# Kernel tuning notes

Hardware: AMD Instinct MI355X
Metric: run time of the kernel (lower is better)

The kernel has to match this reference:

```python
import jax, jax.numpy as jnp
import numpy as np

B, S, D, H = 2, 2048, 1024, 16
DH = D // H
EPS = 1e-5


def _ln(x, g, b):
    m = jnp.mean(x, axis=-1, keepdims=True)
    v = jnp.mean((x - m) ** 2, axis=-1, keepdims=True)
    return (x - m) * jax.lax.rsqrt(v + EPS) * g + b


def setup_inputs() -> dict:
    key = jax.random.key(0)
    ks = jax.random.split(key, 16)
    w = lambda k, shp: jax.random.normal(k, shp, jnp.float32) * 0.02
    return {
        "x": jax.random.normal(ks[0], (B, S, D), jnp.float32),
        # semantic preprocessor: Linear(D,2D) -> ReLU -> Linear(2D,D), residual + LN
        "pW1": w(ks[1], (D, 2 * D)), "pb1": jnp.zeros((2 * D,), jnp.float32),
        "pW2": w(ks[2], (2 * D, D)), "pb2": jnp.zeros((D,), jnp.float32),
        "gp": jnp.ones((D,), jnp.float32), "bp": jnp.zeros((D,), jnp.float32),
        # multi-head attention projections
        "Wq": w(ks[3], (D, D)), "bq": jnp.zeros((D,), jnp.float32),
        "Wk": w(ks[4], (D, D)), "bk": jnp.zeros((D,), jnp.float32),
        "Wv": w(ks[5], (D, D)), "bv": jnp.zeros((D,), jnp.float32),
        "Wo": w(ks[6], (D, D)), "bo": jnp.zeros((D,), jnp.float32),
        "g1": jnp.ones((D,), jnp.float32), "b1": jnp.zeros((D,), jnp.float32),
        # FFN: Linear(D,4D) -> ReLU -> Linear(4D,D)
        "Wf1": w(ks[7], (D, 4 * D)), "bf1": jnp.zeros((4 * D,), jnp.float32),
        "Wf2": w(ks[8], (4 * D, D)), "bf2": jnp.zeros((D,), jnp.float32),
        "g2": jnp.ones((D,), jnp.float32), "b2": jnp.zeros((D,), jnp.float32),
    }


def reference(x, pW1, pb1, pW2, pb2, gp, bp,
              Wq, bq, Wk, bk, Wv, bv, Wo, bo, g1, b1,
              Wf1, bf1, Wf2, bf2, g2, b2):
    # specialized 'semantic' preprocessor (dropout = identity in eval)
    h = jax.nn.relu(x @ pW1 + pb1) @ pW2 + pb2
    s = _ln(x + h, gp, bp)                       # [B,S,D]
    # naive multi-head attention
    q = (s @ Wq + bq).reshape(B, S, H, DH)
    k = (s @ Wk + bk).reshape(B, S, H, DH)
    v = (s @ Wv + bv).reshape(B, S, H, DH)
    scores = jnp.einsum("bqhd,bkhd->bhqk", q, k) / np.sqrt(DH).astype(np.float32)
    attn = jax.nn.softmax(scores, axis=-1)       # [B,H,S,S]
    ctx = jnp.einsum("bhqk,bkhd->bqhd", attn, v).reshape(B, S, D)
    attn_out = ctx @ Wo + bo
    y = _ln(s + attn_out, g1, b1)
    # FFN (dropouts = identity)
    f = jax.nn.relu(y @ Wf1 + bf1) @ Wf2 + bf2
    return _ln(y + f, g2, b2)
```

## Files before the change

kernel.cpp:

```cpp
#include <hip/hip_runtime.h>
#include <cstdint>
#include <cstddef>

typedef _Float16 f16;
typedef _Float16 f16x8 __attribute__((ext_vector_type(8)));
typedef _Float16 f16x4 __attribute__((ext_vector_type(4)));
typedef float    f32x4 __attribute__((ext_vector_type(4)));
typedef float    f32x16 __attribute__((ext_vector_type(16)));

#define MFMA16(a,b,c) __builtin_amdgcn_mfma_f32_16x16x32_f16(a, b, c, 0, 0, 0)
#define MFMA32(a,b,c) __builtin_amdgcn_mfma_f32_32x32x16_f16(a, b, c, 0, 0, 0)

static __device__ __forceinline__ void gload_lds16(const void* g, void* l) {
  __builtin_amdgcn_global_load_lds(
      (const __attribute__((address_space(1))) unsigned int*)g,
      (__attribute__((address_space(3))) unsigned int*)l, 16, 0, 0);
}

static __device__ __forceinline__ int pkh(float a, float b) {
  auto t = __builtin_amdgcn_cvt_pkrtz(a, b);
  return __builtin_bit_cast(int, t);
}

static __device__ __forceinline__ float ex2(float x) {
  return __builtin_amdgcn_exp2f(x);
}

__global__ __launch_bounds__(256) void cast_kernel(const float* __restrict__ x,
                                                   f16* __restrict__ y, int n4) {
  int i = blockIdx.x * 256 + threadIdx.x;
  if (i < n4) {
    float4 v = ((const float4*)x)[i];
    f16x4 h;
    h[0] = (f16)v.x; h[1] = (f16)v.y; h[2] = (f16)v.z; h[3] = (f16)v.w;
    *(f16x4*)(y + (size_t)i * 4) = h;
  }
}

__global__ __launch_bounds__(256) void wtrans(const float* __restrict__ W,
                                              f16* __restrict__ Wt, int K, int N,
                                              float scale) {
  __shared__ float tile[32][33];
  const int n0 = blockIdx.x * 32, k0 = blockIdx.y * 32;
  const int c = threadIdx.x & 31, r = threadIdx.x >> 5;
#pragma unroll
  for (int i = 0; i < 4; i++) {
    int row = r + i * 8;
    tile[row][c] = W[(size_t)(k0 + row) * N + n0 + c];
  }
  __syncthreads();
#pragma unroll
  for (int i = 0; i < 4; i++) {
    int row = r + i * 8;
    Wt[(size_t)(n0 + row) * K + k0 + c] = (f16)(tile[c][row] * scale);
  }
}

__global__ __launch_bounds__(256) void qkvbias_kernel(const float* __restrict__ bq,
                                                      const float* __restrict__ bk,
                                                      const float* __restrict__ bv,
                                                      float* __restrict__ bqkv) {
  int i = blockIdx.x * 256 + threadIdx.x;
  if (i < 1024)       bqkv[i] = bq[i] * 0.18033688f;
  else if (i < 2048)  bqkv[i] = bk[i - 1024];
  else if (i < 3072)  bqkv[i] = bv[i - 2048];
}

template <int MODE, int BN>
__global__ __launch_bounds__(256, 2)
void gemm_kernel(const f16* __restrict__ A, const f16* __restrict__ W,
                 const float* __restrict__ bias, const float* __restrict__ res,
                 void* __restrict__ out, f16* __restrict__ vt, int N, int K) {
  __shared__ __align__(16) f16 lsA[128 * 64];
  __shared__ __align__(16) f16 lsB[BN * 64];
  constexpr int MI = (BN == 128) ? 4 : 2;
  constexpr int NB = (BN == 128) ? 4 : 2;
  const int tid  = threadIdx.x;
  const int lane = tid & 63;
  const int wid  = tid >> 6;
  const int frow = lane & 15;
  const int kgrp = lane >> 4;
  const int wmBase = (BN == 128) ? (wid >> 1) * 64 : wid * 32;
  const int wnBase = (BN == 128) ? (wid & 1) * 64 : 0;
  const int bn = blockIdx.x, bm = blockIdx.y;

  const f32x4 zero4 = {0.f, 0.f, 0.f, 0.f};
  f32x4 acc[MI][4];
#pragma unroll
  for (int i = 0; i < MI; i++)
#pragma unroll
    for (int j = 0; j < 4; j++) acc[i][j] = zero4;

  const f16* aSrc[4]; int lOffA[4];
  const f16* bSrc[NB]; int lOffB[NB];
#pragma unroll
  for (int i = 0; i < 4; i++) {
    int c_lin = i * 256 + wid * 64 + lane;
    int row = c_lin >> 3;
    int ch  = (c_lin & 7) ^ (row & 7);
    aSrc[i] = A + (size_t)(bm * 128 + row) * K + ch * 8;
    lOffA[i] = (i * 256 + wid * 64) * 8;
  }
#pragma unroll
  for (int i = 0; i < NB; i++) {
    int c_lin = i * 256 + wid * 64 + lane;
    int row = c_lin >> 3;
    int ch  = (c_lin & 7) ^ (row & 7);
    bSrc[i] = W + (size_t)(bn * BN + row) * K + ch * 8;
    lOffB[i] = (i * 256 + wid * 64) * 8;
  }

  const int nk = K >> 6;
  for (int ks = 0; ks < nk; ++ks) {
#pragma unroll
    for (int i = 0; i < 4; i++) gload_lds16(aSrc[i] + ks * 64, &lsA[lOffA[i]]);
#pragma unroll
    for (int i = 0; i < NB; i++) gload_lds16(bSrc[i] + ks * 64, &lsB[lOffB[i]]);
    __syncthreads();
#pragma unroll
    for (int kk = 0; kk < 2; kk++) {
      f16x8 af[MI], bf[4];
#pragma unroll
      for (int i = 0; i < MI; i++) {
        int row = wmBase + i * 16 + frow;
        af[i] = *(const f16x8*)&lsA[row * 64 + (((kk * 4 + kgrp) ^ (row & 7)) << 3)];
      }
#pragma unroll
      for (int j = 0; j < 4; j++) {
        int row = wnBase + j * 16 + frow;
        bf[j] = *(const f16x8*)&lsB[row * 64 + (((kk * 4 + kgrp) ^ (row & 7)) << 3)];
      }
#pragma unroll
      for (int i = 0; i < MI; i++)
#pragma unroll
        for (int j = 0; j < 4; j++) acc[i][j] = MFMA16(af[i], bf[j], acc[i][j]);
    }
    __syncthreads();
  }

#pragma unroll
  for (int j = 0; j < 4; j++) {
    const int col = bn * BN + wnBase + j * 16 + frow;
    const float bb = bias[col];
#pragma unroll
    for (int i = 0; i < MI; i++) {
      const int row0 = bm * 128 + wmBase + i * 16 + kgrp * 4;
      if (MODE == 3 && col >= 2048) {
        const int vcol = col - 2048;
        const int bh = (row0 >> 11) * 16 + (vcol >> 6);
        const int d  = vcol & 63;
        const int kv = row0 & 2047;
        f16x4 pk;
#pragma unroll
        for (int r = 0; r < 4; r++) pk[r] = (f16)(acc[i][j][r] + bb);
        *(f16x4*)(vt + ((size_t)bh * 64 + d) * 2048 + kv) = pk;
      } else {
#pragma unroll
        for (int r = 0; r < 4; r++) {
          float v = acc[i][j][r] + bb;
          const size_t idx = (size_t)(row0 + r) * N + col;
          if (MODE == 1) v = fmaxf(v, 0.f);
          if (MODE == 2) ((float*)out)[idx] = v + res[idx];
          else           ((f16*)out)[idx]   = (f16)v;
        }
      }
    }
  }
}

__global__ __launch_bounds__(256, 2)
void attn_kernel(const f16* __restrict__ Qp, const f16* __restrict__ Kp,
                 const f16* __restrict__ Vt, f16* __restrict__ Op, int ldq) {
  __shared__ __align__(16) f16 lsKb[2 * 64 * 64];
  __shared__ __align__(16) f16 lsVb[2 * 64 * 64];
  const int tid = threadIdx.x, lane = tid & 63, wid = tid >> 6;
  const int qcol = lane & 31;
  const int hi = lane >> 5;
  const int bid = blockIdx.x;
  const int bh = ((bid & 7) << 2) | ((bid >> 3) & 3);
  const int qt = bid >> 5;
  const int b = bh >> 4, h = bh & 15;
  const size_t rb = (size_t)b * 2048;
  const int hc = h * 64;
  const int qrow = qt * 128 + wid * 32 + qcol;

  f16x8 qf[4];
  {
    const f16* qp = Qp + (rb + qrow) * ldq + hc;
#pragma unroll
    for (int kc = 0; kc < 4; kc++) qf[kc] = *(const f16x8*)(qp + kc * 16 + hi * 8);
  }

  f32x16 ot0, ot1;
#pragma unroll
  for (int i = 0; i < 16; i++) { ot0[i] = 0.f; ot1[i] = 0.f; }
  float mrun = -1e30f, lrun = 0.f;

  const f16 *kS0, *kS1, *vS0, *vS1;
  int off0, off1;
  {
    int c0 = wid * 64 + lane;
    int r0 = c0 >> 3, ch0 = (c0 & 7) ^ (r0 & 7);
    int c1 = 256 + wid * 64 + lane;
    int r1 = c1 >> 3, ch1 = (c1 & 7) ^ (r1 & 7);
    kS0 = Kp + (rb + r0) * ldq + hc + ch0 * 8;
    kS1 = Kp + (rb + r1) * ldq + hc + ch1 * 8;
    const f16* vbase = Vt + (size_t)bh * 64 * 2048;
    vS0 = vbase + (size_t)r0 * 2048 + ch0 * 8;
    vS1 = vbase + (size_t)r1 * 2048 + ch1 * 8;
    off0 = (wid * 64) * 8;
    off1 = (256 + wid * 64) * 8;
  }

#define STAGE(T, PB)                                                     \
  {                                                                      \
    f16* kd = lsKb + (PB) * 4096;                                        \
    f16* vd = lsVb + (PB) * 4096;                                        \
    const size_t ko = (size_t)(T) * 64 * ldq;                            \
    const size_t vo = (size_t)(T) * 64;                                  \
    gload_lds16(kS0 + ko, kd + off0);                                    \
    gload_lds16(kS1 + ko, kd + off1);                                    \
    gload_lds16(vS0 + vo, vd + off0);                                    \
    gload_lds16(vS1 + vo, vd + off1);                                    \
  }

  STAGE(0, 0);
  asm volatile("s_waitcnt vmcnt(0)" ::: "memory");
  __builtin_amdgcn_s_barrier();

  for (int kt = 0; kt < 32; ++kt) {
    const int cur = kt & 1;
    if (kt < 31) STAGE(kt + 1, cur ^ 1);
    const f16* kb = lsKb + cur * 4096;
    const f16* vb = lsVb + cur * 4096;

#pragma unroll
    for (int st = 0; st < 2; ++st) {
      f32x16 sa;
#pragma unroll
      for (int i = 0; i < 16; i++) sa[i] = 0.f;
      const int krow = st * 32 + qcol;
#pragma unroll
      for (int kc = 0; kc < 4; kc++) {
        f16x8 ak = *(const f16x8*)&kb[krow * 64 + (((kc * 2 + hi) ^ (krow & 7)) << 3)];
        sa = MFMA32(ak, qf[kc], sa);
      }

      float pr[16];
#pragma unroll
      for (int r = 0; r < 16; r++) pr[r] = sa[r];
      float pmax = pr[0];
#pragma unroll
      for (int r = 1; r < 16; r++) pmax = fmaxf(pmax, pr[r]);
      pmax = fmaxf(pmax, __shfl_xor(pmax, 32));
      if (__any(pmax > mrun + 11.54f)) {
        float mn = fmaxf(mrun, pmax);
        float fac = ex2(mrun - mn);
        mrun = mn;
        lrun *= fac;
#pragma unroll
        for (int i = 0; i < 16; i++) { ot0[i] *= fac; ot1[i] *= fac; }
      }
      float ps = 0.f;
#pragma unroll
      for (int r = 0; r < 16; r++) { pr[r] = ex2(pr[r] - mrun); ps += pr[r]; }
      ps += __shfl_xor(ps, 32);
      lrun += ps;

#pragma unroll
      for (int c0 = 0; c0 < 2; c0++) {
        const int c8 = c0 * 8;
        int a0 = pkh(pr[c8 + 0], pr[c8 + 1]);
        int a1 = pkh(pr[c8 + 2], pr[c8 + 3]);
        int b0 = pkh(pr[c8 + 4], pr[c8 + 5]);
        int b1 = pkh(pr[c8 + 6], pr[c8 + 7]);
        int sa0 = __shfl_xor(a0, 32), sb0 = __shfl_xor(b0, 32);
        int sa1 = __shfl_xor(a1, 32), sb1 = __shfl_xor(b1, 32);
        int4 wv;
        wv.x = hi ? sb0 : a0;
        wv.y = hi ? sb1 : a1;
        wv.z = hi ? b0 : sa0;
        wv.w = hi ? b1 : sa1;
        f16x8 pfrag = __builtin_bit_cast(f16x8, wv);
        const int ch = st * 4 + c0 * 2 + hi;
        {
          const int vr = qcol;
          f16x8 av = *(const f16x8*)&vb[vr * 64 + ((ch ^ (vr & 7)) << 3)];
          ot0 = MFMA32(av, pfrag, ot0);
        }
        {
          const int vr = 32 + qcol;
          f16x8 av = *(const f16x8*)&vb[vr * 64 + ((ch ^ (vr & 7)) << 3)];
          ot1 = MFMA32(av, pfrag, ot1);
        }
      }
    }
    asm volatile("s_waitcnt vmcnt(0)" ::: "memory");
    __builtin_amdgcn_s_barrier();
  }
#undef STAGE

  const float rinv = 1.f / lrun;
  f16* op = Op + (rb + qrow) * 1024 + hc;
#pragma unroll
  for (int rr = 0; rr < 16; rr += 2) {
    const int d = (rr & 3) + 8 * (rr >> 2) + 4 * hi;
    *(int*)(op + d)      = pkh(ot0[rr] * rinv, ot0[rr + 1] * rinv);
    *(int*)(op + 32 + d) = pkh(ot1[rr] * rinv, ot1[rr + 1] * rinv);
  }
}

__global__ __launch_bounds__(256)
void ln_kernel(const float* __restrict__ x, const float* __restrict__ g,
               const float* __restrict__ be, float* __restrict__ of,
               f16* __restrict__ ob) {
  const int row = blockIdx.x, t = threadIdx.x;
  const float4 v = ((const float4*)(x + (size_t)row * 1024))[t];
  float s = v.x + v.y + v.z + v.w;
  float q = v.x * v.x + v.y * v.y + v.z * v.z + v.w * v.w;
#pragma unroll
  for (int off = 1; off < 64; off <<= 1) {
    s += __shfl_xor(s, off);
    q += __shfl_xor(q, off);
  }
  __shared__ float ss[4], sq[4];
  if ((t & 63) == 0) { ss[t >> 6] = s; sq[t >> 6] = q; }
  __syncthreads();
  s = ss[0] + ss[1] + ss[2] + ss[3];
  q = sq[0] + sq[1] + sq[2] + sq[3];
  const float mean = s * (1.f / 1024.f);
  const float var  = q * (1.f / 1024.f) - mean * mean;
  const float rstd = rsqrtf(var + 1e-5f);
  const float4 gv = ((const float4*)g)[t];
  const float4 bv = ((const float4*)be)[t];
  float4 ov;
  ov.x = (v.x - mean) * rstd * gv.x + bv.x;
  ov.y = (v.y - mean) * rstd * gv.y + bv.y;
  ov.z = (v.z - mean) * rstd * gv.z + bv.z;
  ov.w = (v.w - mean) * rstd * gv.w + bv.w;
  if (of) ((float4*)(of + (size_t)row * 1024))[t] = ov;
  if (ob) {
    f16x4 hv;
    hv[0] = (f16)ov.x; hv[1] = (f16)ov.y; hv[2] = (f16)ov.z; hv[3] = (f16)ov.w;
    *(f16x4*)(ob + (size_t)row * 1024 + t * 4) = hv;
  }
}

extern "C" void kernel_launch(void* const* d_in, const int* in_sizes, int n_in,
                              void* d_out, int out_size, void* d_ws, size_t ws_size,
                              hipStream_t stream) {
  const float* x   = (const float*)d_in[0];
  const float* pW1 = (const float*)d_in[1];
  const float* pb1 = (const float*)d_in[2];
  const float* pW2 = (const float*)d_in[3];
  const float* pb2 = (const float*)d_in[4];
  const float* gp  = (const float*)d_in[5];
  const float* bp  = (const float*)d_in[6];
  const float* Wq  = (const float*)d_in[7];
  const float* bq  = (const float*)d_in[8];
  const float* Wk  = (const float*)d_in[9];
  const float* bk  = (const float*)d_in[10];
  const float* Wv  = (const float*)d_in[11];
  const float* bv  = (const float*)d_in[12];
  const float* Wo  = (const float*)d_in[13];
  const float* bo  = (const float*)d_in[14];
  const float* g1  = (const float*)d_in[15];
  const float* b1  = (const float*)d_in[16];
  const float* Wf1 = (const float*)d_in[17];
  const float* bf1 = (const float*)d_in[18];
  const float* Wf2 = (const float*)d_in[19];
  const float* bf2 = (const float*)d_in[20];
  const float* g2  = (const float*)d_in[21];
  const float* b2  = (const float*)d_in[22];

  char* ws = (char*)d_ws;
  const size_t MB = 1024 * 1024;
  if (ws_size < 121 * MB) return;

  f16*   wtP1 = (f16*)(ws);
  f16*   wtP2 = (f16*)(ws + 4 * MB);
  f16*   wtQ  = (f16*)(ws + 8 * MB);
  f16*   wtK  = (f16*)(ws + 10 * MB);
  f16*   wtV  = (f16*)(ws + 12 * MB);
  f16*   wtO  = (f16*)(ws + 14 * MB);
  f16*   wtF1 = (f16*)(ws + 16 * MB);
  f16*   wtF2 = (f16*)(ws + 24 * MB);
  f16*   big  = (f16*)(ws + 32 * MB);
  float* t32  = (float*)(ws + 64 * MB);
  float* s32  = (float*)(ws + 80 * MB);
  float* y32  = (float*)(ws + 96 * MB);
  f16*   ybuf = (f16*)(ws + 112 * MB);
  float* bqkv = (float*)(ws + 120 * MB);
  f16* xb  = (f16*)t32;
  f16* sb  = (f16*)y32;
  f16* ctx = ybuf;
  f16* Vt  = big + (size_t)4096 * 3072;

  dim3 blk(256);
  qkvbias_kernel<<<12, blk, 0, stream>>>(bq, bk, bv, bqkv);
  cast_kernel<<<4096, blk, 0, stream>>>(x, xb, 1048576);
  wtrans<<<dim3(64, 32),  blk, 0, stream>>>(pW1, wtP1, 1024, 2048, 1.f);
  wtrans<<<dim3(32, 64),  blk, 0, stream>>>(pW2, wtP2, 2048, 1024, 1.f);
  wtrans<<<dim3(32, 32),  blk, 0, stream>>>(Wq,  wtQ,  1024, 1024, 0.18033688f);
  wtrans<<<dim3(32, 32),  blk, 0, stream>>>(Wk,  wtK,  1024, 1024, 1.f);
  wtrans<<<dim3(32, 32),  blk, 0, stream>>>(Wv,  wtV,  1024, 1024, 1.f);
  wtrans<<<dim3(32, 32),  blk, 0, stream>>>(Wo,  wtO,  1024, 1024, 1.f);
  wtrans<<<dim3(128, 32), blk, 0, stream>>>(Wf1, wtF1, 1024, 4096, 1.f);
  wtrans<<<dim3(32, 128), blk, 0, stream>>>(Wf2, wtF2, 4096, 1024, 1.f);

  gemm_kernel<1,128><<<dim3(16, 32), blk, 0, stream>>>(xb, wtP1, pb1, nullptr, big, nullptr, 2048, 1024);
  gemm_kernel<2,64><<<dim3(16, 32), blk, 0, stream>>>(big, wtP2, pb2, x, t32, nullptr, 1024, 2048);
  ln_kernel<<<4096, blk, 0, stream>>>(t32, gp, bp, s32, sb);
  gemm_kernel<3,128><<<dim3(24, 32), blk, 0, stream>>>(sb, wtQ, bqkv, nullptr, big, Vt, 3072, 1024);
  attn_kernel<<<512, blk, 0, stream>>>(big, big + 1024, Vt, ctx, 3072);
  gemm_kernel<2,64><<<dim3(16, 32), blk, 0, stream>>>(ctx, wtO, bo, s32, t32, nullptr, 1024, 1024);
  ln_kernel<<<4096, blk, 0, stream>>>(t32, g1, b1, y32, ybuf);
  gemm_kernel<1,128><<<dim3(32, 32), blk, 0, stream>>>(ybuf, wtF1, bf1, nullptr, big, nullptr, 4096, 1024);
  gemm_kernel<2,64><<<dim3(16, 32), blk, 0, stream>>>(big, wtF2, bf2, y32, t32, nullptr, 1024, 4096);
  ln_kernel<<<4096, blk, 0, stream>>>(t32, g2, b2, (float*)d_out, nullptr);
}
```

Measured before the change: 321.2 us.

## Double-buffer GEMM LDS loads, deepen attention prefetch, remap workgroups across XCDs

The GEMM kernel now double-buffers its LDS tiles. It issues the global-to-LDS loads for the next K step before computing the current one and uses partial vmcnt waits instead of two full syncthreads per step. The attention kernel moves from two to four K/V LDS buffers with a prefetch distance of two tiles, and MFMA sections are wrapped in s_setprio. GEMM launches switch to a 1D grid whose block index is remapped so that neighbouring tiles land on the same XCD. In exchange, LDS use per block doubles, which may lower occupancy, and redundant tail loads are issued.

```diff
diff --git a/kernel.cpp b/kernel.cpp
--- a/kernel.cpp
+++ b/kernel.cpp
@@ -70,11 +70,12 @@
 __global__ __launch_bounds__(256, 2)
 void gemm_kernel(const f16* __restrict__ A, const f16* __restrict__ W,
                  const float* __restrict__ bias, const float* __restrict__ res,
-                 void* __restrict__ out, f16* __restrict__ vt, int N, int K) {
-  __shared__ __align__(16) f16 lsA[128 * 64];
-  __shared__ __align__(16) f16 lsB[BN * 64];
+                 void* __restrict__ out, f16* __restrict__ vt, int N, int K,
+                 int gx) {
+  constexpr int NB = (BN == 128) ? 4 : 2;
   constexpr int MI = (BN == 128) ? 4 : 2;
-  constexpr int NB = (BN == 128) ? 4 : 2;
+  __shared__ __align__(16) f16 lsA[2 * 128 * 64];
+  __shared__ __align__(16) f16 lsB[2 * BN * 64];
   const int tid  = threadIdx.x;
   const int lane = tid & 63;
   const int wid  = tid >> 6;
@@ -82,7 +83,10 @@
   const int kgrp = lane >> 4;
   const int wmBase = (BN == 128) ? (wid >> 1) * 64 : wid * 32;
   const int wnBase = (BN == 128) ? (wid & 1) * 64 : 0;
-  const int bn = blockIdx.x, bm = blockIdx.y;
+
+  const int nwg = gridDim.x;
+  const int wg = (blockIdx.x & 7) * (nwg >> 3) + (blockIdx.x >> 3);
+  const int bm = wg / gx, bn = wg % gx;
 
   const f32x4 zero4 = {0.f, 0.f, 0.f, 0.f};
   f32x4 acc[MI][4];
@@ -110,33 +114,53 @@
     lOffB[i] = (i * 256 + wid * 64) * 8;
   }
 
+#define GSTAGE(T, PB)                                                     \
+  {                                                                       \
+    f16* la = lsA + (PB) * (128 * 64);                                    \
+    f16* lb = lsB + (PB) * (BN * 64);                                     \
+    _Pragma("unroll") for (int i = 0; i < 4; i++)                         \
+      gload_lds16(aSrc[i] + (size_t)(T) * 64, la + lOffA[i]);             \
+    _Pragma("unroll") for (int i = 0; i < NB; i++)                        \
+      gload_lds16(bSrc[i] + (size_t)(T) * 64, lb + lOffB[i]);             \
+  }
+
   const int nk = K >> 6;
+  GSTAGE(0, 0);
   for (int ks = 0; ks < nk; ++ks) {
-#pragma unroll
-    for (int i = 0; i < 4; i++) gload_lds16(aSrc[i] + ks * 64, &lsA[lOffA[i]]);
-#pragma unroll
-    for (int i = 0; i < NB; i++) gload_lds16(bSrc[i] + ks * 64, &lsB[lOffB[i]]);
-    __syncthreads();
+    const int nt = (ks + 1 < nk) ? ks + 1 : nk - 1;
+    GSTAGE(nt, (ks + 1) & 1);
+    if constexpr (BN == 128)
+      asm volatile("s_waitcnt vmcnt(8)" ::: "memory");
+    else
+      asm volatile("s_waitcnt vmcnt(6)" ::: "memory");
+    __builtin_amdgcn_s_barrier();
+    const f16* la = lsA + (ks & 1) * (128 * 64);
+    const f16* lb = lsB + (ks & 1) * (BN * 64);
 #pragma unroll
     for (int kk = 0; kk < 2; kk++) {
       f16x8 af[MI], bf[4];
 #pragma unroll
       for (int i = 0; i < MI; i++) {
         int row = wmBase + i * 16 + frow;
-        af[i] = *(const f16x8*)&lsA[row * 64 + (((kk * 4 + kgrp) ^ (row & 7)) << 3)];
+        af[i] = *(const f16x8*)&la[row * 64 + (((kk * 4 + kgrp) ^ (row & 7)) << 3)];
       }
 #pragma unroll
       for (int j = 0; j < 4; j++) {
         int row = wnBase + j * 16 + frow;
-        bf[j] = *(const f16x8*)&lsB[row * 64 + (((kk * 4 + kgrp) ^ (row & 7)) << 3)];
-      }
+        bf[j] = *(const f16x8*)&lb[row * 64 + (((kk * 4 + kgrp) ^ (row & 7)) << 3)];
+      }
+      __builtin_amdgcn_s_setprio(1);
 #pragma unroll
       for (int i = 0; i < MI; i++)
 #pragma unroll
         for (int j = 0; j < 4; j++) acc[i][j] = MFMA16(af[i], bf[j], acc[i][j]);
+      __builtin_amdgcn_s_setprio(0);
     }
-    __syncthreads();
-  }
+    asm volatile("" ::: "memory");
+    __builtin_amdgcn_s_barrier();
+  }
+#undef GSTAGE
+  asm volatile("s_waitcnt vmcnt(0)" ::: "memory");
 
 #pragma unroll
   for (int j = 0; j < 4; j++) {
@@ -171,8 +195,8 @@
 __global__ __launch_bounds__(256, 2)
 void attn_kernel(const f16* __restrict__ Qp, const f16* __restrict__ Kp,
                  const f16* __restrict__ Vt, f16* __restrict__ Op, int ldq) {
-  __shared__ __align__(16) f16 lsKb[2 * 64 * 64];
-  __shared__ __align__(16) f16 lsVb[2 * 64 * 64];
+  __shared__ __align__(16) f16 lsKb[4 * 64 * 64];
+  __shared__ __align__(16) f16 lsVb[4 * 64 * 64];
   const int tid = threadIdx.x, lane = tid & 63, wid = tid >> 6;
   const int qcol = lane & 31;
   const int hi = lane >> 5;
@@ -212,7 +236,7 @@
     off1 = (256 + wid * 64) * 8;
   }
 
-#define STAGE(T, PB)                                                     \
+#define ASTAGE(T, PB)                                                    \
   {                                                                      \
     f16* kd = lsKb + (PB) * 4096;                                        \
     f16* vd = lsVb + (PB) * 4096;                                        \
@@ -224,15 +248,16 @@
     gload_lds16(vS1 + vo, vd + off1);                                    \
   }
 
-  STAGE(0, 0);
-  asm volatile("s_waitcnt vmcnt(0)" ::: "memory");
-  __builtin_amdgcn_s_barrier();
+  ASTAGE(0, 0);
+  ASTAGE(1, 1);
 
   for (int kt = 0; kt < 32; ++kt) {
-    const int cur = kt & 1;
-    if (kt < 31) STAGE(kt + 1, cur ^ 1);
-    const f16* kb = lsKb + cur * 4096;
-    const f16* vb = lsVb + cur * 4096;
+    const int t2 = (kt + 2 < 32) ? kt + 2 : 31;
+    ASTAGE(t2, (kt + 2) & 3);
+    asm volatile("s_waitcnt vmcnt(8)" ::: "memory");
+    __builtin_amdgcn_s_barrier();
+    const f16* kb = lsKb + (kt & 3) * 4096;
+    const f16* vb = lsVb + (kt & 3) * 4096;
 
 #pragma unroll
     for (int st = 0; st < 2; ++st) {
@@ -240,11 +265,13 @@
 #pragma unroll
       for (int i = 0; i < 16; i++) sa[i] = 0.f;
       const int krow = st * 32 + qcol;
+      __builtin_amdgcn_s_setprio(1);
 #pragma unroll
       for (int kc = 0; kc < 4; kc++) {
         f16x8 ak = *(const f16x8*)&kb[krow * 64 + (((kc * 2 + hi) ^ (krow & 7)) << 3)];
         sa = MFMA32(ak, qf[kc], sa);
       }
+      __builtin_amdgcn_s_setprio(0);
 
       float pr[16];
 #pragma unroll
@@ -283,22 +310,19 @@
         wv.w = hi ? b1 : sa1;
         f16x8 pfrag = __builtin_bit_cast(f16x8, wv);
         const int ch = st * 4 + c0 * 2 + hi;
-        {
-          const int vr = qcol;
-          f16x8 av = *(const f16x8*)&vb[vr * 64 + ((ch ^ (vr & 7)) << 3)];
-          ot0 = MFMA32(av, pfrag, ot0);
-        }
-        {
-          const int vr = 32 + qcol;
-          f16x8 av = *(const f16x8*)&vb[vr * 64 + ((ch ^ (vr & 7)) << 3)];
-          ot1 = MFMA32(av, pfrag, ot1);
-        }
+        const int vr0 = qcol, vr1 = 32 + qcol;
+        f16x8 av0 = *(const f16x8*)&vb[vr0 * 64 + ((ch ^ (vr0 & 7)) << 3)];
+        f16x8 av1 = *(const f16x8*)&vb[vr1 * 64 + ((ch ^ (vr1 & 7)) << 3)];
+        __builtin_amdgcn_s_setprio(1);
+        ot0 = MFMA32(av0, pfrag, ot0);
+        ot1 = MFMA32(av1, pfrag, ot1);
+        __builtin_amdgcn_s_setprio(0);
       }
     }
-    asm volatile("s_waitcnt vmcnt(0)" ::: "memory");
-    __builtin_amdgcn_s_barrier();
-  }
-#undef STAGE
+    asm volatile("" ::: "memory");
+  }
+#undef ASTAGE
+  asm volatile("s_waitcnt vmcnt(0)" ::: "memory");
 
   const float rinv = 1.f / lrun;
   f16* op = Op + (rb + qrow) * 1024 + hc;
@@ -408,14 +432,14 @@
   wtrans<<<dim3(128, 32), blk, 0, stream>>>(Wf1, wtF1, 1024, 4096, 1.f);
   wtrans<<<dim3(32, 128), blk, 0, stream>>>(Wf2, wtF2, 4096, 1024, 1.f);
 
-  gemm_kernel<1,128><<<dim3(16, 32), blk, 0, stream>>>(xb, wtP1, pb1, nullptr, big, nullptr, 2048, 1024);
-  gemm_kernel<2,64><<<dim3(16, 32), blk, 0, stream>>>(big, wtP2, pb2, x, t32, nullptr, 1024, 2048);
+  gemm_kernel<1,128><<<512, blk, 0, stream>>>(xb, wtP1, pb1, nullptr, big, nullptr, 2048, 1024, 16);
+  gemm_kernel<2,64><<<512, blk, 0, stream>>>(big, wtP2, pb2, x, t32, nullptr, 1024, 2048, 16);
   ln_kernel<<<4096, blk, 0, stream>>>(t32, gp, bp, s32, sb);
-  gemm_kernel<3,128><<<dim3(24, 32), blk, 0, stream>>>(sb, wtQ, bqkv, nullptr, big, Vt, 3072, 1024);
+  gemm_kernel<3,128><<<768, blk, 0, stream>>>(sb, wtQ, bqkv, nullptr, big, Vt, 3072, 1024, 24);
   attn_kernel<<<512, blk, 0, stream>>>(big, big + 1024, Vt, ctx, 3072);
-  gemm_kernel<2,64><<<dim3(16, 32), blk, 0, stream>>>(ctx, wtO, bo, s32, t32, nullptr, 1024, 1024);
+  gemm_kernel<2,64><<<512, blk, 0, stream>>>(ctx, wtO, bo, s32, t32, nullptr, 1024, 1024, 16);
   ln_kernel<<<4096, blk, 0, stream>>>(t32, g1, b1, y32, ybuf);
-  gemm_kernel<1,128><<<dim3(32, 32), blk, 0, stream>>>(ybuf, wtF1, bf1, nullptr, big, nullptr, 4096, 1024);
-  gemm_kernel<2,64><<<dim3(16, 32), blk, 0, stream>>>(big, wtF2, bf2, y32, t32, nullptr, 1024, 4096);
+  gemm_kernel<1,128><<<1024, blk, 0, stream>>>(ybuf, wtF1, bf1, nullptr, big, nullptr, 4096, 1024, 32);
+  gemm_kernel<2,64><<<512, blk, 0, stream>>>(big, wtF2, bf2, y32, t32, nullptr, 1024, 4096, 16);
   ln_kernel<<<4096, blk, 0, stream>>>(t32, g2, b2, (float*)d_out, nullptr);
 }
```

Measured after the change: 335.3 us. 1.04x slower.

## Split attention KV range in two with log-sum-exp combine kernel

Applied to the files above, without the earlier changes.

Each (batch, head, q-tile) attention block now covers half of the key/value sequence, doubling the grid to 1024 blocks. Each half writes a normalized partial output plus a log2-sum-exp value, and a new combine kernel merges the two halves into ctx. The inner loop also computes both 32-row score tiles before a single softmax update, replaces the xor-32 shuffles with permlane32_swap, raises MFMA priority with s_setprio, and allows 4 blocks per CU. The aim is better CU occupancy and fewer cross-lane ops, at the cost of an extra kernel launch and extra global traffic for the partial outputs.

```diff
diff --git a/kernel.cpp b/kernel.cpp
--- a/kernel.cpp
+++ b/kernel.cpp
@@ -7,6 +7,7 @@
 typedef _Float16 f16x4 __attribute__((ext_vector_type(4)));
 typedef float    f32x4 __attribute__((ext_vector_type(4)));
 typedef float    f32x16 __attribute__((ext_vector_type(16)));
+typedef unsigned int uint2v __attribute__((ext_vector_type(2)));
 
 #define MFMA16(a,b,c) __builtin_amdgcn_mfma_f32_16x16x32_f16(a, b, c, 0, 0, 0)
 #define MFMA32(a,b,c) __builtin_amdgcn_mfma_f32_32x32x16_f16(a, b, c, 0, 0, 0)
@@ -24,6 +25,18 @@
 
 static __device__ __forceinline__ float ex2(float x) {
   return __builtin_amdgcn_exp2f(x);
+}
+
+static __device__ __forceinline__ uint2v pswap(int a, int b) {
+  return __builtin_amdgcn_permlane32_swap((unsigned)a, (unsigned)b, false, false);
+}
+static __device__ __forceinline__ float xhalf_max(float x) {
+  uint2v r = pswap(__builtin_bit_cast(int, x), __builtin_bit_cast(int, x));
+  return fmaxf(__builtin_bit_cast(float, r.x), __builtin_bit_cast(float, r.y));
+}
+static __device__ __forceinline__ float xhalf_sum(float x) {
+  uint2v r = pswap(__builtin_bit_cast(int, x), __builtin_bit_cast(int, x));
+  return __builtin_bit_cast(float, r.x) + __builtin_bit_cast(float, r.y);
 }
 
 __global__ __launch_bounds__(256) void cast_kernel(const float* __restrict__ x,
@@ -168,20 +181,25 @@
   }
 }
 
-__global__ __launch_bounds__(256, 2)
+__global__ __launch_bounds__(256, 4)
 void attn_kernel(const f16* __restrict__ Qp, const f16* __restrict__ Kp,
-                 const f16* __restrict__ Vt, f16* __restrict__ Op, int ldq) {
+                 const f16* __restrict__ Vt, f16* __restrict__ opart,
+                 float* __restrict__ Lbuf, int ldq) {
   __shared__ __align__(16) f16 lsKb[2 * 64 * 64];
   __shared__ __align__(16) f16 lsVb[2 * 64 * 64];
   const int tid = threadIdx.x, lane = tid & 63, wid = tid >> 6;
   const int qcol = lane & 31;
   const int hi = lane >> 5;
   const int bid = blockIdx.x;
-  const int bh = ((bid & 7) << 2) | ((bid >> 3) & 3);
-  const int qt = bid >> 5;
+  const int idx = bid >> 3;
+  const int bh = ((bid & 7) << 2) | (idx & 3);
+  const int rest = idx >> 2;
+  const int part = rest & 1;
+  const int qt = rest >> 1;
   const int b = bh >> 4, h = bh & 15;
   const size_t rb = (size_t)b * 2048;
   const int hc = h * 64;
+  const int kv0 = part * 1024;
   const int qrow = qt * 128 + wid * 32 + qcol;
 
   f16x8 qf[4];
@@ -203,16 +221,16 @@
     int r0 = c0 >> 3, ch0 = (c0 & 7) ^ (r0 & 7);
     int c1 = 256 + wid * 64 + lane;
     int r1 = c1 >> 3, ch1 = (c1 & 7) ^ (r1 & 7);
-    kS0 = Kp + (rb + r0) * ldq + hc + ch0 * 8;
-    kS1 = Kp + (rb + r1) * ldq + hc + ch1 * 8;
-    const f16* vbase = Vt + (size_t)bh * 64 * 2048;
+    kS0 = Kp + (rb + kv0 + r0) * ldq + hc + ch0 * 8;
+    kS1 = Kp + (rb + kv0 + r1) * ldq + hc + ch1 * 8;
+    const f16* vbase = Vt + (size_t)bh * 64 * 2048 + kv0;
     vS0 = vbase + (size_t)r0 * 2048 + ch0 * 8;
     vS1 = vbase + (size_t)r1 * 2048 + ch1 * 8;
     off0 = (wid * 64) * 8;
     off1 = (256 + wid * 64) * 8;
   }
 
-#define STAGE(T, PB)                                                     \
+#define ASTAGE(T, PB)                                                    \
   {                                                                      \
     f16* kd = lsKb + (PB) * 4096;                                        \
     f16* vd = lsVb + (PB) * 4096;                                        \
@@ -224,90 +242,135 @@
     gload_lds16(vS1 + vo, vd + off1);                                    \
   }
 
-  STAGE(0, 0);
+  ASTAGE(0, 0);
   asm volatile("s_waitcnt vmcnt(0)" ::: "memory");
   __builtin_amdgcn_s_barrier();
 
-  for (int kt = 0; kt < 32; ++kt) {
+  for (int kt = 0; kt < 16; ++kt) {
     const int cur = kt & 1;
-    if (kt < 31) STAGE(kt + 1, cur ^ 1);
+    if (kt < 15) ASTAGE(kt + 1, cur ^ 1);
     const f16* kb = lsKb + cur * 4096;
     const f16* vb = lsVb + cur * 4096;
 
+    f32x16 s0, s1;
+#pragma unroll
+    for (int i = 0; i < 16; i++) { s0[i] = 0.f; s1[i] = 0.f; }
+    const int kr0 = qcol, kr1 = 32 + qcol;
+    __builtin_amdgcn_s_setprio(1);
+#pragma unroll
+    for (int kc = 0; kc < 4; kc++) {
+      f16x8 a0 = *(const f16x8*)&kb[kr0 * 64 + (((kc * 2 + hi) ^ (kr0 & 7)) << 3)];
+      f16x8 a1 = *(const f16x8*)&kb[kr1 * 64 + (((kc * 2 + hi) ^ (kr1 & 7)) << 3)];
+      s0 = MFMA32(a0, qf[kc], s0);
+      s1 = MFMA32(a1, qf[kc], s1);
+    }
+    __builtin_amdgcn_s_setprio(0);
+
+    float mx[16];
+#pragma unroll
+    for (int r = 0; r < 16; r++) mx[r] = fmaxf(s0[r], s1[r]);
+#pragma unroll
+    for (int w = 8; w > 0; w >>= 1)
+#pragma unroll
+      for (int r = 0; r < w; r++) mx[r] = fmaxf(mx[r], mx[r + w]);
+    float pmax = xhalf_max(mx[0]);
+    if (__any(pmax > mrun + 11.54f)) {
+      float mn = fmaxf(mrun, pmax);
+      float fac = ex2(mrun - mn);
+      mrun = mn;
+      lrun *= fac;
+#pragma unroll
+      for (int i = 0; i < 16; i++) { ot0[i] *= fac; ot1[i] *= fac; }
+    }
+#pragma unroll
+    for (int r = 0; r < 16; r++) {
+      s0[r] = ex2(s0[r] - mrun);
+      s1[r] = ex2(s1[r] - mrun);
+    }
+    float sm[16];
+#pragma unroll
+    for (int r = 0; r < 16; r++) sm[r] = s0[r] + s1[r];
+#pragma unroll
+    for (int w = 8; w > 0; w >>= 1)
+#pragma unroll
+      for (int r = 0; r < w; r++) sm[r] += sm[r + w];
+    lrun += xhalf_sum(sm[0]);
+
 #pragma unroll
     for (int st = 0; st < 2; ++st) {
-      f32x16 sa;
-#pragma unroll
-      for (int i = 0; i < 16; i++) sa[i] = 0.f;
-      const int krow = st * 32 + qcol;
-#pragma unroll
-      for (int kc = 0; kc < 4; kc++) {
-        f16x8 ak = *(const f16x8*)&kb[krow * 64 + (((kc * 2 + hi) ^ (krow & 7)) << 3)];
-        sa = MFMA32(ak, qf[kc], sa);
-      }
-
-      float pr[16];
-#pragma unroll
-      for (int r = 0; r < 16; r++) pr[r] = sa[r];
-      float pmax = pr[0];
-#pragma unroll
-      for (int r = 1; r < 16; r++) pmax = fmaxf(pmax, pr[r]);
-      pmax = fmaxf(pmax, __shfl_xor(pmax, 32));
-      if (__any(pmax > mrun + 11.54f)) {
-        float mn = fmaxf(mrun, pmax);
-        float fac = ex2(mrun - mn);
-        mrun = mn;
-        lrun *= fac;
-#pragma unroll
-        for (int i = 0; i < 16; i++) { ot0[i] *= fac; ot1[i] *= fac; }
-      }
-      float ps = 0.f;
-#pragma unroll
-      for (int r = 0; r < 16; r++) { pr[r] = ex2(pr[r] - mrun); ps += pr[r]; }
-      ps += __shfl_xor(ps, 32);
-      lrun += ps;
-
 #pragma unroll
       for (int c0 = 0; c0 < 2; c0++) {
         const int c8 = c0 * 8;
-        int a0 = pkh(pr[c8 + 0], pr[c8 + 1]);
-        int a1 = pkh(pr[c8 + 2], pr[c8 + 3]);
-        int b0 = pkh(pr[c8 + 4], pr[c8 + 5]);
-        int b1 = pkh(pr[c8 + 6], pr[c8 + 7]);
-        int sa0 = __shfl_xor(a0, 32), sb0 = __shfl_xor(b0, 32);
-        int sa1 = __shfl_xor(a1, 32), sb1 = __shfl_xor(b1, 32);
+        int a0, a1, b0, b1;
+        if (st == 0) {
+          a0 = pkh(s0[c8 + 0], s0[c8 + 1]); a1 = pkh(s0[c8 + 2], s0[c8 + 3]);
+          b0 = pkh(s0[c8 + 4], s0[c8 + 5]); b1 = pkh(s0[c8 + 6], s0[c8 + 7]);
+        } else {
+          a0 = pkh(s1[c8 + 0], s1[c8 + 1]); a1 = pkh(s1[c8 + 2], s1[c8 + 3]);
+          b0 = pkh(s1[c8 + 4], s1[c8 + 5]); b1 = pkh(s1[c8 + 6], s1[c8 + 7]);
+        }
+        uint2v r0 = pswap(a0, b0);
+        uint2v r1 = pswap(a1, b1);
         int4 wv;
-        wv.x = hi ? sb0 : a0;
-        wv.y = hi ? sb1 : a1;
-        wv.z = hi ? b0 : sa0;
-        wv.w = hi ? b1 : sa1;
+        wv.x = (int)r0.x; wv.y = (int)r1.x; wv.z = (int)r0.y; wv.w = (int)r1.y;
         f16x8 pfrag = __builtin_bit_cast(f16x8, wv);
         const int ch = st * 4 + c0 * 2 + hi;
-        {
-          const int vr = qcol;
-          f16x8 av = *(const f16x8*)&vb[vr * 64 + ((ch ^ (vr & 7)) << 3)];
-          ot0 = MFMA32(av, pfrag, ot0);
-        }
-        {
-          const int vr = 32 + qcol;
-          f16x8 av = *(const f16x8*)&vb[vr * 64 + ((ch ^ (vr & 7)) << 3)];
-          ot1 = MFMA32(av, pfrag, ot1);
-        }
+        const int vr0 = qcol, vr1 = 32 + qcol;
+        f16x8 av0 = *(const f16x8*)&vb[vr0 * 64 + ((ch ^ (vr0 & 7)) << 3)];
+        f16x8 av1 = *(const f16x8*)&vb[vr1 * 64 + ((ch ^ (vr1 & 7)) << 3)];
+        __builtin_amdgcn_s_setprio(1);
+        ot0 = MFMA32(av0, pfrag, ot0);
+        ot1 = MFMA32(av1, pfrag, ot1);
+        __builtin_amdgcn_s_setprio(0);
       }
     }
     asm volatile("s_waitcnt vmcnt(0)" ::: "memory");
     __builtin_amdgcn_s_barrier();
   }
-#undef STAGE
+#undef ASTAGE
 
   const float rinv = 1.f / lrun;
-  f16* op = Op + (rb + qrow) * 1024 + hc;
+  const size_t pbase = ((size_t)part * 32 + bh) * 2048 + qrow;
+  f16* pp = opart + pbase * 64;
 #pragma unroll
   for (int rr = 0; rr < 16; rr += 2) {
     const int d = (rr & 3) + 8 * (rr >> 2) + 4 * hi;
-    *(int*)(op + d)      = pkh(ot0[rr] * rinv, ot0[rr + 1] * rinv);
-    *(int*)(op + 32 + d) = pkh(ot1[rr] * rinv, ot1[rr + 1] * rinv);
-  }
+    *(int*)(pp + d)      = pkh(ot0[rr] * rinv, ot0[rr + 1] * rinv);
+    *(int*)(pp + 32 + d) = pkh(ot1[rr] * rinv, ot1[rr + 1] * rinv);
+  }
+  if (hi == 0) Lbuf[pbase] = mrun + __builtin_amdgcn_logf(lrun);
+}
+
+__global__ __launch_bounds__(256)
+void combine_kernel(const f16* __restrict__ opart, const float* __restrict__ Lbuf,
+                    f16* __restrict__ ctx) {
+  const int bid = blockIdx.x;
+  const int bh = bid >> 5, qblk = bid & 31;
+  const int t = threadIdx.x;
+  const int q = qblk * 64 + (t >> 2);
+  const int dp = (t & 3) * 16;
+  const size_t base = (size_t)bh * 2048 + q;
+  const size_t p1o = (size_t)32 * 2048;
+  const float L0 = Lbuf[base];
+  const float L1 = Lbuf[p1o + base];
+  const float L = fmaxf(L0, L1);
+  float w0 = ex2(L0 - L), w1 = ex2(L1 - L);
+  const float rs = 1.f / (w0 + w1);
+  w0 *= rs; w1 *= rs;
+  const f16* p0 = opart + base * 64 + dp;
+  const f16* p1 = opart + (p1o + base) * 64 + dp;
+  f16x8 a0 = *(const f16x8*)p0, a1 = *(const f16x8*)(p0 + 8);
+  f16x8 c0 = *(const f16x8*)p1, c1 = *(const f16x8*)(p1 + 8);
+  f16x8 o0, o1;
+#pragma unroll
+  for (int j = 0; j < 8; j++) {
+    o0[j] = (f16)(w0 * (float)a0[j] + w1 * (float)c0[j]);
+    o1[j] = (f16)(w0 * (float)a1[j] + w1 * (float)c1[j]);
+  }
+  const int b = bh >> 4, h = bh & 15;
+  f16* op = ctx + ((size_t)b * 2048 + q) * 1024 + h * 64 + dp;
+  *(f16x8*)op = o0;
+  *(f16x8*)(op + 8) = o1;
 }
 
 __global__ __launch_bounds__(256)
@@ -391,10 +454,12 @@
   float* y32  = (float*)(ws + 96 * MB);
   f16*   ybuf = (f16*)(ws + 112 * MB);
   float* bqkv = (float*)(ws + 120 * MB);
-  f16* xb  = (f16*)t32;
-  f16* sb  = (f16*)y32;
-  f16* ctx = ybuf;
-  f16* Vt  = big + (size_t)4096 * 3072;
+  f16* xb    = (f16*)t32;
+  f16* sb    = (f16*)y32;
+  f16* ctx   = ybuf;
+  f16* Vt    = big + (size_t)4096 * 3072;
+  f16* opart = (f16*)y32;
+  float* Lbuf = t32;
 
   dim3 blk(256);
   qkvbias_kernel<<<12, blk, 0, stream>>>(bq, bk, bv, bqkv);
@@ -412,7 +477,8 @@
   gemm_kernel<2,64><<<dim3(16, 32), blk, 0, stream>>>(big, wtP2, pb2, x, t32, nullptr, 1024, 2048);
   ln_kernel<<<4096, blk, 0, stream>>>(t32, gp, bp, s32, sb);
   gemm_kernel<3,128><<<dim3(24, 32), blk, 0, stream>>>(sb, wtQ, bqkv, nullptr, big, Vt, 3072, 1024);
-  attn_kernel<<<512, blk, 0, stream>>>(big, big + 1024, Vt, ctx, 3072);
+  attn_kernel<<<1024, blk, 0, stream>>>(big, big + 1024, Vt, opart, Lbuf, 3072);
+  combine_kernel<<<1024, blk, 0, stream>>>(opart, Lbuf, ctx);
   gemm_kernel<2,64><<<dim3(16, 32), blk, 0, stream>>>(ctx, wtO, bo, s32, t32, nullptr, 1024, 1024);
   ln_kernel<<<4096, blk, 0, stream>>>(t32, g1, b1, y32, ybuf);
   gemm_kernel<1,128><<<dim3(32, 32), blk, 0, stream>>>(ybuf, wtF1, bf1, nullptr, big, nullptr, 4096, 1024);
```

Measured after the change: 320.5 us. Within noise of the previous version (-0.2%).
